# Kernel tuning notes

Hardware: AMD Instinct MI355X
Metric: run time of the kernel (lower is better)

## Reference

```python
import jax, jax.numpy as jnp
import numpy as np

S, B, D, K, E = 2048, 16, 256, 2048, 1048576  # seq_len, batch, input_dim, max_seq_len, n_edges


def setup_inputs() -> dict:
    key = jax.random.key(0)
    k1, k2, k3, k4, k5 = jax.random.split(key, 5)
    M = jax.random.normal(k1, (S, B, D), dtype=jnp.float32)
    W = jax.random.normal(k2, (K, D), dtype=jnp.float32) * (1.0 / np.sqrt(D))
    lengths = jax.random.randint(k3, (B,), 1, S, dtype=jnp.int64)
    edge_batch = jax.random.randint(k4, (E,), 0, B, dtype=jnp.int64)
    edge_ij = jax.random.randint(k5, (E, 2), 0, K, dtype=jnp.int64)
    return {"M": M, "W": W, "lengths": lengths, "edge_batch": edge_batch, "edge_ij": edge_ij}


def reference(M, W, lengths, edge_batch, edge_ij):
    # scale = Linear(input_dim, max_seq_len, bias=False): (S, B, K)
    scale = jnp.einsum('sbd,kd->sbk', M, W)
    # softmax over the sequence dim (dim=0), then permute(1,2,0) -> (B, K, S)
    alpha = jnp.transpose(jax.nn.softmax(scale, axis=0), (1, 2, 0))
    # mask = ones*1e-10 with edges set to 1; mask_copy = zeros with edges set to 1
    mask = jnp.full(alpha.shape, 1e-10, dtype=alpha.dtype)
    mask = mask.at[edge_batch, edge_ij[:, 0], edge_ij[:, 1]].set(1.0)
    mask_copy = jnp.zeros(alpha.shape, dtype=alpha.dtype)
    mask_copy = mask_copy.at[edge_batch, edge_ij[:, 0], edge_ij[:, 1]].set(1.0)
    masked_alpha = alpha * mask
    sums = masked_alpha.sum(-1, keepdims=True)
    scores = (masked_alpha / sums) * mask_copy
    return scores
```

## Files before the change

### kernel.cpp

```cpp
#include <hip/hip_runtime.h>

#define S_LEN 2048
#define B_DIM 16
#define D_DIM 256
#define K_DIM 2048
#define E_NUM 1048576

typedef __attribute__((ext_vector_type(4))) float f32x4;
typedef __attribute__((ext_vector_type(8))) short s16x8;
typedef __attribute__((ext_vector_type(4))) unsigned short u16x4;
typedef __attribute__((ext_vector_type(8))) unsigned short u16x8;

__device__ __forceinline__ unsigned short f2bf(float f) {
    unsigned int u = __float_as_uint(f);
    u += 0x7fffu + ((u >> 16) & 1u);
    return (unsigned short)(u >> 16);
}

__global__ void prep_kernel(const float* __restrict__ W, const float* __restrict__ M,
                            unsigned short* __restrict__ Wbf, unsigned short* __restrict__ Mbf,
                            unsigned long long* __restrict__ mw) {
    int bid = blockIdx.x;
    if (bid < 2048) {
        int t = bid * 256 + threadIdx.x;
        ((f32x4*)mw)[t] = (f32x4){0.f, 0.f, 0.f, 0.f};
    } else if (bid < 2560) {
        int t = (bid - 2048) * 256 + threadIdx.x;
        f32x4 v = ((const f32x4*)W)[t];
        u16x4 u;
        u.x = f2bf(v.x); u.y = f2bf(v.y); u.z = f2bf(v.z); u.w = f2bf(v.w);
        ((u16x4*)Wbf)[t] = u;
    } else {
        int t = (bid - 2560) * 256 + threadIdx.x;
        f32x4 v = ((const f32x4*)M)[t];
        int flat4 = t * 4;
        int d0 = flat4 & 255;
        int sb = flat4 >> 8;
        int b  = sb & 15;
        int s  = sb >> 4;
        u16x4 u;
        u.x = f2bf(v.x); u.y = f2bf(v.y); u.z = f2bf(v.z); u.w = f2bf(v.w);
        *(u16x4*)&Mbf[((size_t)(b * S_LEN + s)) * D_DIM + d0] = u;
    }
}

__global__ void maskbuild_kernel(const int* __restrict__ eb, const int* __restrict__ ij,
                                 unsigned long long* __restrict__ mw) {
    int e = blockIdx.x * 256 + threadIdx.x;
    int b = eb[e];
    int2 p = *(const int2*)&ij[2 * e];
    size_t w = ((size_t)(b * K_DIM + p.x)) * 32 + (p.y >> 6);
    atomicOr(&mw[w], 1ull << (p.y & 63));
}

__launch_bounds__(512, 2)
__global__ void gemm5_kernel(const unsigned short* __restrict__ Mbf,
                             const unsigned short* __restrict__ Wbf,
                             const unsigned long long* __restrict__ mw,
                             float* __restrict__ out) {
    __shared__ unsigned short Msh[2][64 * 256];
    __shared__ float smZ[8][2][16];
    __shared__ float smE[8][2][16];

    const int tid  = threadIdx.x;
    const int x    = blockIdx.x;
    const int b    = ((x & 7) << 1) | ((x >> 3) & 1);
    const int k0   = (x >> 4) * 128;
    const int lane = tid & 63;
    const int w    = tid >> 6;
    const int wk   = w & 3;
    const int ws   = w >> 2;
    const int r    = lane & 15;
    const int g    = lane >> 4;

    const unsigned short* MB = Mbf + (size_t)b * S_LEN * D_DIM;
    const int kc0 = k0 + wk * 32 + r;
    const size_t orow0 = (size_t)(b * K_DIM + kc0) * S_LEN;
    const size_t mrow0 = (size_t)(b * K_DIM + kc0) * 32;

    s16x8 breg[2][8];
    #pragma unroll
    for (int ks = 0; ks < 2; ++ks)
        #pragma unroll
        for (int d = 0; d < 8; ++d)
            breg[ks][d] = *(const s16x8*)&Wbf[(size_t)(kc0 + ks * 16) * D_DIM + d * 32 + g * 8];

    const int lrh  = lane >> 5;
    const int lc16 = lane & 31;

    auto stage = [&](int bufi, int t) {
        const int s0 = t * 64;
        #pragma unroll
        for (int c = 0; c < 4; ++c) {
            const int row   = w * 8 + c * 2 + lrh;
            const int col16 = lc16 ^ (row & 7);
            const unsigned short* src = MB + (size_t)(s0 + row) * D_DIM + col16 * 8;
            char* dst = (char*)(&Msh[bufi][0]) + w * 4096 + c * 1024;
            __builtin_amdgcn_global_load_lds(
                (__attribute__((address_space(1))) const void*)src,
                (__attribute__((address_space(3))) void*)dst, 16, 0, 0);
        }
    };

    float Zl[2]  = {0.f, 0.f};
    float Zel[2] = {0.f, 0.f};

    stage(0, 0);
    unsigned long long wn0 = mw[mrow0], wn1 = mw[mrow0 + 512];
    __syncthreads();

    for (int t = 0; t < 32; ++t) {
        if (t < 31) stage((t & 1) ^ 1, t + 1);
        const unsigned long long wv0 = wn0, wv1 = wn1;
        if (t < 31) { wn0 = mw[mrow0 + t + 1]; wn1 = mw[mrow0 + 512 + t + 1]; }
        const unsigned short* cur = &Msh[t & 1][0];

        f32x4 acc[2][2];
        #pragma unroll
        for (int q = 0; q < 2; ++q)
            #pragma unroll
            for (int ks = 0; ks < 2; ++ks) acc[q][ks] = (f32x4){0.f, 0.f, 0.f, 0.f};

        #pragma unroll
        for (int d = 0; d < 8; ++d) {
            const int acol = ((d * 4 + g) ^ (r & 7)) * 8;
            #pragma unroll
            for (int q = 0; q < 2; ++q) {
                s16x8 a = *(const s16x8*)&cur[(ws * 32 + q * 16 + r) * 256 + acol];
                acc[q][0] = __builtin_amdgcn_mfma_f32_16x16x32_bf16(a, breg[0][d], acc[q][0], 0, 0, 0);
                acc[q][1] = __builtin_amdgcn_mfma_f32_16x16x32_bf16(a, breg[1][d], acc[q][1], 0, 0, 0);
            }
        }

        #pragma unroll
        for (int q = 0; q < 2; ++q) {
            const int sh = ws * 32 + q * 16 + g * 4;
            #pragma unroll
            for (int rr = 0; rr < 4; ++rr) {
                float e0 = __expf(acc[q][0][rr]);
                float e1 = __expf(acc[q][1][rr]);
                Zl[0] += e0; Zl[1] += e1;
                Zel[0] += ((wv0 >> (sh + rr)) & 1ull) ? e0 : 0.f;
                Zel[1] += ((wv1 >> (sh + rr)) & 1ull) ? e1 : 0.f;
            }
        }
        __syncthreads();
    }

    #pragma unroll
    for (int ks = 0; ks < 2; ++ks) {
        Zl[ks]  += __shfl_xor(Zl[ks], 16);  Zl[ks]  += __shfl_xor(Zl[ks], 32);
        Zel[ks] += __shfl_xor(Zel[ks], 16); Zel[ks] += __shfl_xor(Zel[ks], 32);
    }
    if (g == 0) {
        smZ[w][0][r] = Zl[0]; smZ[w][1][r] = Zl[1];
        smE[w][0][r] = Zel[0]; smE[w][1][r] = Zel[1];
    }
    __syncthreads();
    float rdv[2];
    #pragma unroll
    for (int ks = 0; ks < 2; ++ks) {
        float Z  = Zl[ks]  + smZ[w ^ 4][ks][r];
        float Ze = Zel[ks] + smE[w ^ 4][ks][r];
        rdv[ks] = 1.0f / (1e-10f * (Z - Ze) + Ze);
    }

    stage(0, 0);
    wn0 = mw[mrow0]; wn1 = mw[mrow0 + 512];
    __syncthreads();

    for (int t = 0; t < 32; ++t) {
        if (t < 31) stage((t & 1) ^ 1, t + 1);
        const unsigned long long wv0 = wn0, wv1 = wn1;
        if (t < 31) { wn0 = mw[mrow0 + t + 1]; wn1 = mw[mrow0 + 512 + t + 1]; }
        const unsigned short* cur = &Msh[t & 1][0];

        f32x4 acc[2][2];
        #pragma unroll
        for (int q = 0; q < 2; ++q)
            #pragma unroll
            for (int ks = 0; ks < 2; ++ks) acc[q][ks] = (f32x4){0.f, 0.f, 0.f, 0.f};

        #pragma unroll
        for (int d = 0; d < 8; ++d) {
            const int acol = ((d * 4 + g) ^ (r & 7)) * 8;
            #pragma unroll
            for (int q = 0; q < 2; ++q) {
                s16x8 a = *(const s16x8*)&cur[(ws * 32 + q * 16 + r) * 256 + acol];
                acc[q][0] = __builtin_amdgcn_mfma_f32_16x16x32_bf16(a, breg[0][d], acc[q][0], 0, 0, 0);
                acc[q][1] = __builtin_amdgcn_mfma_f32_16x16x32_bf16(a, breg[1][d], acc[q][1], 0, 0, 0);
            }
        }

        #pragma unroll
        for (int q = 0; q < 2; ++q) {
            const int sh = ws * 32 + q * 16 + g * 4;
            const size_t so = (size_t)(t * 64 + ws * 32 + q * 16 + g * 4);
            #pragma unroll
            for (int ks = 0; ks < 2; ++ks) {
                const unsigned long long bits = ks ? wv1 : wv0;
                f32x4 ov;
                #pragma unroll
                for (int rr = 0; rr < 4; ++rr) {
                    bool edge = (bits >> (sh + rr)) & 1ull;
                    ov[rr] = edge ? __expf(acc[q][ks][rr]) * rdv[ks] : 0.f;
                }
                __builtin_nontemporal_store(ov,
                    (f32x4*)&out[orow0 + (size_t)ks * 16 * S_LEN + so]);
            }
        }
        __syncthreads();
    }
}

extern "C" void kernel_launch(void* const* d_in, const int* in_sizes, int n_in,
                              void* d_out, int out_size, void* d_ws, size_t ws_size,
                              hipStream_t stream) {
    (void)in_sizes; (void)n_in; (void)ws_size; (void)out_size;
    const float* M  = (const float*)d_in[0];
    const float* W  = (const float*)d_in[1];
    const int* eb   = (const int*)d_in[3];
    const int* ij   = (const int*)d_in[4];
    float* out      = (float*)d_out;
    char* ws        = (char*)d_ws;

    unsigned long long* mw = (unsigned long long*)ws;
    unsigned short* Wbf = (unsigned short*)(ws + 8388608);
    unsigned short* Mbf = (unsigned short*)(ws + 9437184);

    prep_kernel<<<10752, 256, 0, stream>>>(W, M, Wbf, Mbf, mw);
    maskbuild_kernel<<<E_NUM / 256, 256, 0, stream>>>(eb, ij, mw);
    gemm5_kernel<<<256, 512, 0, stream>>>(Mbf, Wbf, mw, out);
}
```

Measured before the change: 204.7 us.

## Stage output tiles through LDS for coalesced 512B row stores, halve block size

Each block now covers 64 K-rows instead of 128, with 256 threads and twice as many blocks. In the second pass, softmax outputs are written to a swizzled LDS tile covering two 64-column steps, then stored to global as contiguous 512-byte row segments instead of scattered 16-byte stores. The LDS output tile also serves as the second staging buffer in the first pass, and mask words are loaded directly rather than prefetched. The trade-offs are that the second pass loses double-buffered prefetch and gains an extra barrier per step, and each block reloads all of M while sharing it across fewer K rows.

```diff
diff --git a/kernel.cpp b/kernel.cpp
--- a/kernel.cpp
+++ b/kernel.cpp
@@ -9,7 +9,6 @@
 typedef __attribute__((ext_vector_type(4))) float f32x4;
 typedef __attribute__((ext_vector_type(8))) short s16x8;
 typedef __attribute__((ext_vector_type(4))) unsigned short u16x4;
-typedef __attribute__((ext_vector_type(8))) unsigned short u16x8;
 
 __device__ __forceinline__ unsigned short f2bf(float f) {
     unsigned int u = __float_as_uint(f);
@@ -53,29 +52,29 @@
     atomicOr(&mw[w], 1ull << (p.y & 63));
 }
 
-__launch_bounds__(512, 2)
-__global__ void gemm5_kernel(const unsigned short* __restrict__ Mbf,
+__launch_bounds__(256, 2)
+__global__ void gemm6_kernel(const unsigned short* __restrict__ Mbf,
                              const unsigned short* __restrict__ Wbf,
                              const unsigned long long* __restrict__ mw,
                              float* __restrict__ out) {
-    __shared__ unsigned short Msh[2][64 * 256];
-    __shared__ float smZ[8][2][16];
-    __shared__ float smE[8][2][16];
+    __shared__ unsigned short Msh[64 * 256];
+    __shared__ float sc[64 * 128];
+    __shared__ float smZ[4][2][16];
+    __shared__ float smE[4][2][16];
 
     const int tid  = threadIdx.x;
     const int x    = blockIdx.x;
     const int b    = ((x & 7) << 1) | ((x >> 3) & 1);
-    const int k0   = (x >> 4) * 128;
+    const int k0   = (x >> 4) * 64;
     const int lane = tid & 63;
     const int w    = tid >> 6;
-    const int wk   = w & 3;
-    const int ws   = w >> 2;
+    const int wk   = w & 1;
+    const int ws   = w >> 1;
     const int r    = lane & 15;
     const int g    = lane >> 4;
 
     const unsigned short* MB = Mbf + (size_t)b * S_LEN * D_DIM;
     const int kc0 = k0 + wk * 32 + r;
-    const size_t orow0 = (size_t)(b * K_DIM + kc0) * S_LEN;
     const size_t mrow0 = (size_t)(b * K_DIM + kc0) * 32;
 
     s16x8 breg[2][8];
@@ -90,12 +89,13 @@
 
     auto stage = [&](int bufi, int t) {
         const int s0 = t * 64;
-        #pragma unroll
-        for (int c = 0; c < 4; ++c) {
-            const int row   = w * 8 + c * 2 + lrh;
+        unsigned short* buf = bufi ? (unsigned short*)sc : Msh;
+        #pragma unroll
+        for (int c = 0; c < 8; ++c) {
+            const int row   = w * 16 + c * 2 + lrh;
             const int col16 = lc16 ^ (row & 7);
             const unsigned short* src = MB + (size_t)(s0 + row) * D_DIM + col16 * 8;
-            char* dst = (char*)(&Msh[bufi][0]) + w * 4096 + c * 1024;
+            char* dst = (char*)buf + w * 8192 + c * 1024;
             __builtin_amdgcn_global_load_lds(
                 (__attribute__((address_space(1))) const void*)src,
                 (__attribute__((address_space(3))) void*)dst, 16, 0, 0);
@@ -106,14 +106,13 @@
     float Zel[2] = {0.f, 0.f};
 
     stage(0, 0);
-    unsigned long long wn0 = mw[mrow0], wn1 = mw[mrow0 + 512];
     __syncthreads();
 
     for (int t = 0; t < 32; ++t) {
         if (t < 31) stage((t & 1) ^ 1, t + 1);
-        const unsigned long long wv0 = wn0, wv1 = wn1;
-        if (t < 31) { wn0 = mw[mrow0 + t + 1]; wn1 = mw[mrow0 + 512 + t + 1]; }
-        const unsigned short* cur = &Msh[t & 1][0];
+        const unsigned long long wv0 = mw[mrow0 + t];
+        const unsigned long long wv1 = mw[mrow0 + 512 + t];
+        const unsigned short* cur = (t & 1) ? (const unsigned short*)sc : Msh;
 
         f32x4 acc[2][2];
         #pragma unroll
@@ -147,6 +146,8 @@
         __syncthreads();
     }
 
+    stage(0, 0);
+
     #pragma unroll
     for (int ks = 0; ks < 2; ++ks) {
         Zl[ks]  += __shfl_xor(Zl[ks], 16);  Zl[ks]  += __shfl_xor(Zl[ks], 32);
@@ -160,20 +161,15 @@
     float rdv[2];
     #pragma unroll
     for (int ks = 0; ks < 2; ++ks) {
-        float Z  = Zl[ks]  + smZ[w ^ 4][ks][r];
-        float Ze = Zel[ks] + smE[w ^ 4][ks][r];
+        float Z  = Zl[ks]  + smZ[w ^ 2][ks][r];
+        float Ze = Zel[ks] + smE[w ^ 2][ks][r];
         rdv[ks] = 1.0f / (1e-10f * (Z - Ze) + Ze);
     }
 
-    stage(0, 0);
-    wn0 = mw[mrow0]; wn1 = mw[mrow0 + 512];
-    __syncthreads();
-
     for (int t = 0; t < 32; ++t) {
-        if (t < 31) stage((t & 1) ^ 1, t + 1);
-        const unsigned long long wv0 = wn0, wv1 = wn1;
-        if (t < 31) { wn0 = mw[mrow0 + t + 1]; wn1 = mw[mrow0 + 512 + t + 1]; }
-        const unsigned short* cur = &Msh[t & 1][0];
+        const int h = t & 1;
+        const unsigned long long wv0 = mw[mrow0 + t];
+        const unsigned long long wv1 = mw[mrow0 + 512 + t];
 
         f32x4 acc[2][2];
         #pragma unroll
@@ -186,7 +182,7 @@
             const int acol = ((d * 4 + g) ^ (r & 7)) * 8;
             #pragma unroll
             for (int q = 0; q < 2; ++q) {
-                s16x8 a = *(const s16x8*)&cur[(ws * 32 + q * 16 + r) * 256 + acol];
+                s16x8 a = *(const s16x8*)&Msh[(ws * 32 + q * 16 + r) * 256 + acol];
                 acc[q][0] = __builtin_amdgcn_mfma_f32_16x16x32_bf16(a, breg[0][d], acc[q][0], 0, 0, 0);
                 acc[q][1] = __builtin_amdgcn_mfma_f32_16x16x32_bf16(a, breg[1][d], acc[q][1], 0, 0, 0);
             }
@@ -195,21 +191,35 @@
         #pragma unroll
         for (int q = 0; q < 2; ++q) {
             const int sh = ws * 32 + q * 16 + g * 4;
-            const size_t so = (size_t)(t * 64 + ws * 32 + q * 16 + g * 4);
             #pragma unroll
             for (int ks = 0; ks < 2; ++ks) {
                 const unsigned long long bits = ks ? wv1 : wv0;
-                f32x4 ov;
+                const int row = wk * 32 + ks * 16 + r;
+                const int colb = h * 64 + ws * 32 + q * 16 + g * 4;
+                const int phys = ((colb >> 2) ^ (row & 31));
+                f32x4 v;
                 #pragma unroll
                 for (int rr = 0; rr < 4; ++rr) {
                     bool edge = (bits >> (sh + rr)) & 1ull;
-                    ov[rr] = edge ? __expf(acc[q][ks][rr]) * rdv[ks] : 0.f;
+                    v[rr] = edge ? __expf(acc[q][ks][rr]) * rdv[ks] : 0.f;
                 }
-                __builtin_nontemporal_store(ov,
-                    (f32x4*)&out[orow0 + (size_t)ks * 16 * S_LEN + so]);
+                *(f32x4*)&sc[row * 128 + phys * 4] = v;
             }
         }
         __syncthreads();
+
+        if (t < 31) stage(0, t + 1);
+        if (h) {
+            const int sg = t >> 1;
+            const int slot = lane & 31;
+            #pragma unroll
+            for (int i = 0; i < 8; ++i) {
+                const int row = w * 16 + i * 2 + lrh;
+                f32x4 v = *(const f32x4*)&sc[row * 128 + (slot ^ (row & 31)) * 4];
+                *(f32x4*)&out[(size_t)(b * K_DIM + k0 + row) * S_LEN + sg * 128 + slot * 4] = v;
+            }
+        }
+        if (t < 31) __syncthreads();
     }
 }
 
@@ -230,5 +240,5 @@
 
     prep_kernel<<<10752, 256, 0, stream>>>(W, M, Wbf, Mbf, mw);
     maskbuild_kernel<<<E_NUM / 256, 256, 0, stream>>>(eb, ij, mw);
-    gemm5_kernel<<<256, 512, 0, stream>>>(Mbf, Wbf, mw, out);
-}
+    gemm6_kernel<<<512, 256, 0, stream>>>(Mbf, Wbf, mw, out);
+}
```

Result: faster. 176.4 us (-13.8%).

## Single GEMM pass writing unnormalized exp, rescale edge entries in finalize kernel

Applied to the files above, without the earlier changes.

Drops the first GEMM pass that only computed the softmax normalizers. The kernel now writes masked exp values while accumulating the row sums in the same pass, stores the reciprocal normalizer per row, and a new finalize kernel rescales only the set edge positions by walking the bitmask. This halves the MFMA work and M staging, at the cost of an extra launch and scattered read-modify-write on the roughly one million edge outputs. The output stores also switch from nontemporal to ordinary stores.

```diff
diff --git a/kernel.cpp b/kernel.cpp
--- a/kernel.cpp
+++ b/kernel.cpp
@@ -9,7 +9,6 @@
 typedef __attribute__((ext_vector_type(4))) float f32x4;
 typedef __attribute__((ext_vector_type(8))) short s16x8;
 typedef __attribute__((ext_vector_type(4))) unsigned short u16x4;
-typedef __attribute__((ext_vector_type(8))) unsigned short u16x8;
 
 __device__ __forceinline__ unsigned short f2bf(float f) {
     unsigned int u = __float_as_uint(f);
@@ -54,10 +53,11 @@
 }
 
 __launch_bounds__(512, 2)
-__global__ void gemm5_kernel(const unsigned short* __restrict__ Mbf,
-                             const unsigned short* __restrict__ Wbf,
-                             const unsigned long long* __restrict__ mw,
-                             float* __restrict__ out) {
+__global__ void gemm13_kernel(const unsigned short* __restrict__ Mbf,
+                              const unsigned short* __restrict__ Wbf,
+                              const unsigned long long* __restrict__ mw,
+                              float* __restrict__ rd,
+                              float* __restrict__ out) {
     __shared__ unsigned short Msh[2][64 * 256];
     __shared__ float smZ[8][2][16];
     __shared__ float smE[8][2][16];
@@ -90,12 +90,13 @@
 
     auto stage = [&](int bufi, int t) {
         const int s0 = t * 64;
+        unsigned short* buf = &Msh[bufi][0];
         #pragma unroll
         for (int c = 0; c < 4; ++c) {
             const int row   = w * 8 + c * 2 + lrh;
             const int col16 = lc16 ^ (row & 7);
             const unsigned short* src = MB + (size_t)(s0 + row) * D_DIM + col16 * 8;
-            char* dst = (char*)(&Msh[bufi][0]) + w * 4096 + c * 1024;
+            char* dst = (char*)buf + w * 4096 + c * 1024;
             __builtin_amdgcn_global_load_lds(
                 (__attribute__((address_space(1))) const void*)src,
                 (__attribute__((address_space(3))) void*)dst, 16, 0, 0);
@@ -107,66 +108,6 @@
 
     stage(0, 0);
     unsigned long long wn0 = mw[mrow0], wn1 = mw[mrow0 + 512];
-    __syncthreads();
-
-    for (int t = 0; t < 32; ++t) {
-        if (t < 31) stage((t & 1) ^ 1, t + 1);
-        const unsigned long long wv0 = wn0, wv1 = wn1;
-        if (t < 31) { wn0 = mw[mrow0 + t + 1]; wn1 = mw[mrow0 + 512 + t + 1]; }
-        const unsigned short* cur = &Msh[t & 1][0];
-
-        f32x4 acc[2][2];
-        #pragma unroll
-        for (int q = 0; q < 2; ++q)
-            #pragma unroll
-            for (int ks = 0; ks < 2; ++ks) acc[q][ks] = (f32x4){0.f, 0.f, 0.f, 0.f};
-
-        #pragma unroll
-        for (int d = 0; d < 8; ++d) {
-            const int acol = ((d * 4 + g) ^ (r & 7)) * 8;
-            #pragma unroll
-            for (int q = 0; q < 2; ++q) {
-                s16x8 a = *(const s16x8*)&cur[(ws * 32 + q * 16 + r) * 256 + acol];
-                acc[q][0] = __builtin_amdgcn_mfma_f32_16x16x32_bf16(a, breg[0][d], acc[q][0], 0, 0, 0);
-                acc[q][1] = __builtin_amdgcn_mfma_f32_16x16x32_bf16(a, breg[1][d], acc[q][1], 0, 0, 0);
-            }
-        }
-
-        #pragma unroll
-        for (int q = 0; q < 2; ++q) {
-            const int sh = ws * 32 + q * 16 + g * 4;
-            #pragma unroll
-            for (int rr = 0; rr < 4; ++rr) {
-                float e0 = __expf(acc[q][0][rr]);
-                float e1 = __expf(acc[q][1][rr]);
-                Zl[0] += e0; Zl[1] += e1;
-                Zel[0] += ((wv0 >> (sh + rr)) & 1ull) ? e0 : 0.f;
-                Zel[1] += ((wv1 >> (sh + rr)) & 1ull) ? e1 : 0.f;
-            }
-        }
-        __syncthreads();
-    }
-
-    #pragma unroll
-    for (int ks = 0; ks < 2; ++ks) {
-        Zl[ks]  += __shfl_xor(Zl[ks], 16);  Zl[ks]  += __shfl_xor(Zl[ks], 32);
-        Zel[ks] += __shfl_xor(Zel[ks], 16); Zel[ks] += __shfl_xor(Zel[ks], 32);
-    }
-    if (g == 0) {
-        smZ[w][0][r] = Zl[0]; smZ[w][1][r] = Zl[1];
-        smE[w][0][r] = Zel[0]; smE[w][1][r] = Zel[1];
-    }
-    __syncthreads();
-    float rdv[2];
-    #pragma unroll
-    for (int ks = 0; ks < 2; ++ks) {
-        float Z  = Zl[ks]  + smZ[w ^ 4][ks][r];
-        float Ze = Zel[ks] + smE[w ^ 4][ks][r];
-        rdv[ks] = 1.0f / (1e-10f * (Z - Ze) + Ze);
-    }
-
-    stage(0, 0);
-    wn0 = mw[mrow0]; wn1 = mw[mrow0 + 512];
     __syncthreads();
 
     for (int t = 0; t < 32; ++t) {
@@ -202,14 +143,52 @@
                 f32x4 ov;
                 #pragma unroll
                 for (int rr = 0; rr < 4; ++rr) {
+                    float e = __expf(acc[q][ks][rr]);
+                    Zl[ks] += e;
                     bool edge = (bits >> (sh + rr)) & 1ull;
-                    ov[rr] = edge ? __expf(acc[q][ks][rr]) * rdv[ks] : 0.f;
+                    Zel[ks] += edge ? e : 0.f;
+                    ov[rr] = edge ? e : 0.f;
                 }
-                __builtin_nontemporal_store(ov,
-                    (f32x4*)&out[orow0 + (size_t)ks * 16 * S_LEN + so]);
+                *(f32x4*)&out[orow0 + (size_t)ks * 16 * S_LEN + so] = ov;
             }
         }
         __syncthreads();
+    }
+
+    #pragma unroll
+    for (int ks = 0; ks < 2; ++ks) {
+        Zl[ks]  += __shfl_xor(Zl[ks], 16);  Zl[ks]  += __shfl_xor(Zl[ks], 32);
+        Zel[ks] += __shfl_xor(Zel[ks], 16); Zel[ks] += __shfl_xor(Zel[ks], 32);
+    }
+    if (g == 0) {
+        smZ[w][0][r] = Zl[0]; smZ[w][1][r] = Zl[1];
+        smE[w][0][r] = Zel[0]; smE[w][1][r] = Zel[1];
+    }
+    __syncthreads();
+    if (ws == 0 && g == 0) {
+        #pragma unroll
+        for (int ks = 0; ks < 2; ++ks) {
+            float Z  = Zl[ks]  + smZ[w ^ 4][ks][r];
+            float Ze = Zel[ks] + smE[w ^ 4][ks][r];
+            rd[b * K_DIM + k0 + wk * 32 + ks * 16 + r] =
+                1.0f / (1e-10f * (Z - Ze) + Ze);
+        }
+    }
+}
+
+__global__ void finalize_kernel(const unsigned long long* __restrict__ mw,
+                                const float* __restrict__ rd,
+                                float* __restrict__ out) {
+    int t = blockIdx.x * 256 + threadIdx.x;
+    unsigned long long bits = mw[t];
+    if (!bits) return;
+    const int row = t >> 5;
+    const float rdv = rd[row];
+    const size_t base = (size_t)row * S_LEN + (t & 31) * 64;
+    while (bits) {
+        const int j = __builtin_ctzll(bits);
+        bits &= bits - 1;
+        out[base + j] *= rdv;
     }
 }
 
@@ -227,8 +206,10 @@
     unsigned long long* mw = (unsigned long long*)ws;
     unsigned short* Wbf = (unsigned short*)(ws + 8388608);
     unsigned short* Mbf = (unsigned short*)(ws + 9437184);
+    float* rd = (float*)(ws + 26214400);
 
     prep_kernel<<<10752, 256, 0, stream>>>(W, M, Wbf, Mbf, mw);
     maskbuild_kernel<<<E_NUM / 256, 256, 0, stream>>>(eb, ij, mw);
-    gemm5_kernel<<<256, 512, 0, stream>>>(Mbf, Wbf, mw, out);
-}
+    gemm13_kernel<<<256, 512, 0, stream>>>(Mbf, Wbf, mw, rd, out);
+    finalize_kernel<<<4096, 256, 0, stream>>>(mw, rd, out);
+}
```

After: 177.0 us. 1.16x faster.
